# Performance work log

Measured on AMD Instinct MI355X. Metric: run time of the kernel, lower is better.

## Reference

```python
import jax, jax.numpy as jnp
import numpy as np

B, S, D = 64, 14, 2048   # batch, enc_image_size, encoder_dim
A, H, E = 512, 512, 512  # attention_dim, lstm_size, embedding_size
V, L = 10000, 20         # vocab_size, max caption length (T = L-1 decode steps)


def setup_inputs() -> dict:
    key = jax.random.key(0)
    ks = jax.random.split(key, 24)
    p = lambda k, shape: jax.random.normal(k, shape, jnp.float32) * 0.02
    features = jax.random.normal(ks[0], (B, S, S, D), jnp.float32)
    captions = jax.random.randint(ks[1], (B, L), 0, V)
    # sorted descending lengths in [2, L], max forced to L so T_dec = L-1
    lengths = jnp.sort(jax.random.randint(ks[2], (B,), 2, L + 1))[::-1]
    lengths = lengths.at[0].set(L)
    return {
        'features': features, 'captions': captions, 'lengths': lengths,
        'emb': p(ks[3], (V, E)),
        'W_ih': p(ks[4], (4 * H, D + E)), 'b_ih': p(ks[5], (4 * H,)),
        'W_hh': p(ks[6], (4 * H, H)), 'b_hh': p(ks[7], (4 * H,)),
        'h_fc_w': p(ks[8], (H, D)), 'h_fc_b': p(ks[9], (H,)),
        'c_fc_w': p(ks[10], (H, D)), 'c_fc_b': p(ks[11], (H,)),
        'f_beta_w': p(ks[12], (D, H)), 'f_beta_b': p(ks[13], (D,)),
        'cls_w': p(ks[14], (V, H)), 'cls_b': p(ks[15], (V,)),
        'enc_w': p(ks[16], (A, D)), 'enc_b': p(ks[17], (A,)),
        'dec_w': p(ks[18], (A, H)), 'dec_b': p(ks[19], (A,)),
        'att_w': p(ks[20], (1, A)), 'att_b': p(ks[21], (1,)),
    }


def reference(features, captions, lengths, emb, W_ih, b_ih, W_hh, b_hh,
              h_fc_w, h_fc_b, c_fc_w, c_fc_b, f_beta_w, f_beta_b,
              cls_w, cls_b, enc_w, enc_b, dec_w, dec_b, att_w, att_b):
    feats = features.reshape(features.shape[0], -1, features.shape[-1])  # (B,P,D)
    emb_seq = emb[captions]                                              # (B,L,E)
    mean_f = feats.mean(axis=1)
    h = mean_f @ h_fc_w.T + h_fc_b
    c = mean_f @ c_fc_w.T + c_fc_b
    dec_len = lengths - 1
    T = captions.shape[1] - 1
    # attention encoder projection is time-invariant: hoist out of the loop
    att1 = jnp.einsum('bpd,ad->bpa', feats, enc_w) + enc_b               # (B,P,A)

    def step(carry, xs):
        h, c = carry
        x_emb, t = xs
        att2 = h @ dec_w.T + dec_b                                       # (B,A)
        e = jnp.einsum('bpa,a->bp', jax.nn.relu(att1 + att2[:, None, :]), att_w[0]) + att_b[0]
        alpha = jax.nn.softmax(e, axis=1)                                # (B,P)
        awe = jnp.einsum('bp,bpd->bd', alpha, feats)
        gate = jax.nn.sigmoid(h @ f_beta_w.T + f_beta_b)
        awe = gate * awe
        x = jnp.concatenate([x_emb, awe], axis=1)                        # (B,E+D)
        gates = x @ W_ih.T + b_ih + h @ W_hh.T + b_hh                    # torch gate order i,f,g,o
        i, f, g, o = jnp.split(gates, 4, axis=1)
        c2 = jax.nn.sigmoid(f) * c + jax.nn.sigmoid(i) * jnp.tanh(g)
        h2 = jax.nn.sigmoid(o) * jnp.tanh(c2)
        y = h2 @ cls_w.T + cls_b                                         # dropout = eval identity
        active = (t < dec_len)[:, None]
        return (h2, c2), (jnp.where(active, y, 0.0), jnp.where(active, alpha, 0.0))

    xs = (jnp.swapaxes(emb_seq[:, :T], 0, 1), jnp.arange(T))
    (_, _), (y_pred, alphas) = jax.lax.scan(step, (h, c), xs)
    return jnp.swapaxes(y_pred, 0, 1), jnp.swapaxes(alphas, 0, 1)
```

## Files before the change

kernel.cpp:

```cpp
#include <hip/hip_runtime.h>
#include <math.h>

typedef __attribute__((ext_vector_type(8))) short bf16x8;
typedef __attribute__((ext_vector_type(8))) unsigned short u16x8;
typedef __attribute__((ext_vector_type(4))) float f32x4;

#define NB 64
#define NP 196
#define ND 2048
#define NA 512
#define NH 512
#define NE 512
#define NV 10000
#define NT 19
#define NKX 3072
#define NROW (NB*NP)
#define NVP 10112
#define MROW 1280
#define PP 200

__device__ __forceinline__ unsigned short f2bu(float f){
    unsigned int u; __builtin_memcpy(&u, &f, 4);
    u = (u + 0x7FFFu + ((u >> 16) & 1u)) >> 16;
    return (unsigned short)u;
}
__device__ __forceinline__ float b2f(short s){
    unsigned int u = ((unsigned int)(unsigned short)s) << 16;
    float f; __builtin_memcpy(&f, &u, 4); return f;
}
__device__ __forceinline__ float sigm(float x){ return 1.f/(1.f + __expf(-x)); }

__device__ __forceinline__ void gll16(const void* g, void* l){
    __builtin_amdgcn_global_load_lds(
        (const __attribute__((address_space(1))) void*)g,
        (__attribute__((address_space(3))) void*)l, 16, 0, 0);
}


__global__ void k_cast4(const float4* __restrict__ src, ushort4* __restrict__ dst, int n4){
    int stride = gridDim.x * blockDim.x;
    for (int i = blockIdx.x*blockDim.x + threadIdx.x; i < n4; i += stride){
        float4 v = src[i];
        ushort4 o = { f2bu(v.x), f2bu(v.y), f2bu(v.z), f2bu(v.w) };
        dst[i] = o;
    }
}

__global__ void k_wcat(const float* __restrict__ wih, const float* __restrict__ whh,
                       unsigned short* __restrict__ wcat){
    int j = blockIdx.x;
    int k = blockIdx.y*256 + threadIdx.x;
    float v = (k < 2560) ? wih[j*2560 + k] : whh[j*512 + (k - 2560)];
    wcat[j*NKX + k] = f2bu(v);
}

__global__ void k_tr(const float* __restrict__ feats,
                     unsigned short* __restrict__ fbf,
                     unsigned short* __restrict__ ftr,
                     float* __restrict__ meanf){
    __shared__ unsigned short sm[64][202];
    __shared__ float rsum[256];
    int dt = blockIdx.x;
    int b  = blockIdx.y;
    int tid = threadIdx.x;
    int d = tid & 63;
    int gd = dt*64 + d;
    float s = 0.f;
    for (int p = (tid >> 6); p < NP; p += 4){
        float v = feats[((size_t)(b*NP + p))*ND + gd];
        unsigned short u = f2bu(v);
        fbf[((size_t)(b*NP + p))*ND + gd] = u;
        sm[d][p] = u;
        s += v;
    }
    rsum[tid] = s;
    __syncthreads();
    if (tid < 64)
        meanf[b*ND + dt*64 + tid] =
            (rsum[tid] + rsum[tid+64] + rsum[tid+128] + rsum[tid+192]) * (1.f/196.f);
    for (int v = tid; v < 64*25; v += 256){
        int r = v/25, c = v - r*25;
        u16x8 o;
        #pragma unroll
        for (int j = 0; j < 8; j++){ int p = c*8 + j; o[j] = (p < NP) ? sm[r][p] : (unsigned short)0; }
        *(u16x8*)(ftr + ((size_t)(b*ND + dt*64 + r))*PP + c*8) = o;
    }
}

__global__ void k_hc0(const float* __restrict__ meanf,
                      const float* __restrict__ hw, const float* __restrict__ hb,
                      const float* __restrict__ cw, const float* __restrict__ cb,
                      unsigned short* __restrict__ hbf, float* __restrict__ cst){
    int sel = blockIdx.y;
    const float* wmat = sel ? cw : hw;
    const float* bias = sel ? cb : hb;
    int jg = blockIdx.x;
    int tid = threadIdx.x;
    int b = tid & 63, jj = tid >> 6;
    int j = jg*4 + jj;
    __shared__ float ml[64][33];
    __shared__ float wl[4][32];
    float acc = 0.f;
    for (int kc = 0; kc < ND; kc += 32){
        __syncthreads();
        #pragma unroll
        for (int q = 0; q < 8; q++){
            int lin = tid + q*256;
            int r = lin >> 5, kk = lin & 31;
            ml[r][kk] = meanf[r*ND + kc + kk];
        }
        if (tid < 128){ int r = tid >> 5, kk = tid & 31; wl[r][kk] = wmat[(jg*4 + r)*ND + kc + kk]; }
        __syncthreads();
        #pragma unroll
        for (int kk = 0; kk < 32; kk++) acc += ml[b][kk] * wl[jj][kk];
    }
    acc += bias[j];
    if (sel) cst[b*NH + j] = acc;
    else     hbf[b*NH + j] = f2bu(acc);
}

template<int K>
__device__ __forceinline__ void gemm128(const unsigned short* __restrict__ A,
                                        const unsigned short* __restrict__ B,
                                        int brow, int bcol, f32x4 acc[4][4]){
    __shared__ unsigned short As[128*32];
    __shared__ unsigned short Bs[128*32];
    int tid = threadIdx.x;
    int w = tid >> 6, l = tid & 63;
    int wr = (w >> 1) * 64, wc = (w & 1) * 64;
    int lr = l & 15, kg = (l >> 4) * 8;
    const unsigned short* ga0 = A + (size_t)(brow + (tid >> 2))*K + (tid & 3)*8;
    const unsigned short* gb0 = B + (size_t)(bcol + (tid >> 2))*K + (tid & 3)*8;
    for (int k0 = 0; k0 < K; k0 += 32){
        __syncthreads();
        gll16(ga0 + k0,            As + w*512);
        gll16(ga0 + (size_t)64*K + k0, As + 2048 + w*512);
        gll16(gb0 + k0,            Bs + w*512);
        gll16(gb0 + (size_t)64*K + k0, Bs + 2048 + w*512);
        __syncthreads();
        bf16x8 af[4], bfr[4];
        #pragma unroll
        for (int mi = 0; mi < 4; mi++)
            af[mi] = *(const bf16x8*)(As + (wr + mi*16 + lr)*32 + kg);
        #pragma unroll
        for (int ni = 0; ni < 4; ni++)
            bfr[ni] = *(const bf16x8*)(Bs + (wc + ni*16 + lr)*32 + kg);
        #pragma unroll
        for (int ni = 0; ni < 4; ni++){
            #pragma unroll
            for (int mi = 0; mi < 4; mi++)
                acc[mi][ni] = __builtin_amdgcn_mfma_f32_16x16x32_bf16(af[mi], bfr[ni], acc[mi][ni], 0, 0, 0);
        }
    }
}

__global__ void k_gemm_att1(const unsigned short* __restrict__ fbf,
                            const unsigned short* __restrict__ encw,
                            const float* __restrict__ enc_b,
                            unsigned short* __restrict__ att1){
    f32x4 acc[4][4] = {};
    int brow = blockIdx.x*128, bcol = blockIdx.y*128;
    gemm128<ND>(fbf, encw, brow, bcol, acc);
    int w = threadIdx.x >> 6, l = threadIdx.x & 63;
    int wr = (w >> 1) * 64, wc = (w & 1) * 64;
    int r0 = brow + wr + (l >> 4)*4;
    int c0 = bcol + wc + (l & 15);
    #pragma unroll
    for (int ni = 0; ni < 4; ni++){
        int col = c0 + ni*16;
        float eb = enc_b[col];
        #pragma unroll
        for (int mi = 0; mi < 4; mi++){
            #pragma unroll
            for (int r = 0; r < 4; r++)
                att1[(size_t)(r0 + mi*16 + r)*NA + col] = f2bu(acc[mi][ni][r] + eb);
        }
    }
}

__global__ void k_gemm_cls(const unsigned short* __restrict__ hsb,
                           const unsigned short* __restrict__ clsw,
                           const float* __restrict__ cls_b,
                           const int* __restrict__ lengths,
                           float* __restrict__ yout){
    f32x4 acc[4][4] = {};
    int brow = blockIdx.x*128, bcol = blockIdx.y*128;
    gemm128<NH>(hsb, clsw, brow, bcol, acc);
    int w = threadIdx.x >> 6, l = threadIdx.x & 63;
    int wr = (w >> 1) * 64, wc = (w & 1) * 64;
    int r0 = brow + wr + (l >> 4)*4;
    int c0 = bcol + wc + (l & 15);
    #pragma unroll
    for (int ni = 0; ni < 4; ni++){
        int col = c0 + ni*16;
        if (col >= NV) continue;
        float cb = cls_b[col];
        #pragma unroll
        for (int mi = 0; mi < 4; mi++){
            #pragma unroll
            for (int r = 0; r < 4; r++){
                int grow = r0 + mi*16 + r;
                if (grow >= NT*64) continue;
                int t = grow >> 6, bb = grow & 63;
                int active = t < (lengths[bb] - 1);
                yout[((size_t)bb*NT + t)*NV + col] = active ? (acc[mi][ni][r] + cb) : 0.f;
            }
        }
    }
}


__global__ void k_hproj(const unsigned short* __restrict__ hbf,
                        const unsigned short* __restrict__ hwb,
                        float* __restrict__ hp){
    int w = threadIdx.x >> 6, l = threadIdx.x & 63;
    int nt = blockIdx.x;
    int row = 16*w + (l & 15);
    int col = nt*16 + (l & 15);
    int kg = (l >> 4) * 8;
    f32x4 acc = {};
    for (int k0 = 0; k0 < NH; k0 += 32){
        bf16x8 af = *(const bf16x8*)(hbf + row*NH + k0 + kg);
        bf16x8 bv = *(const bf16x8*)(hwb + col*NH + k0 + kg);
        acc = __builtin_amdgcn_mfma_f32_16x16x32_bf16(af, bv, acc, 0, 0, 0);
    }
    int r0 = 16*w + (l >> 4)*4;
    #pragma unroll
    for (int r = 0; r < 4; r++)
        hp[(r0 + r)*2560 + col] = acc[r];
}

__global__ void k_e(const unsigned short* __restrict__ att1,
                    const float* __restrict__ hp, const float* __restrict__ dec_b,
                    const float* __restrict__ att_w, const float* __restrict__ att_b,
                    const float* __restrict__ emb, const int* __restrict__ captions,
                    const unsigned short* __restrict__ hbf,
                    unsigned short* __restrict__ xh, float* __restrict__ ews, int t){
    __shared__ float at2[NA];
    __shared__ float aw[NA];
    int b = blockIdx.x >> 2, pc = blockIdx.x & 3;
    int tid = threadIdx.x;
    for (int j = tid; j < NA; j += 256){
        at2[j] = hp[b*2560 + j] + dec_b[j];
        aw[j]  = att_w[j];
    }
    if (pc == 0){
        int cap = captions[b*20 + t];
        for (int k = tid; k < NE; k += 256) xh[b*NKX + k] = f2bu(emb[cap*NE + k]);
        for (int j = tid; j < NH; j += 256) xh[b*NKX + 2560 + j] = hbf[b*NH + j];
    }
    __syncthreads();
    int pl = tid >> 2, q = tid & 3;
    if (pl < 49){
        int p = pc*49 + pl;
        const unsigned short* arow = att1 + ((size_t)(b*NP + p))*NA + q*128;
        float s = 0.f;
        for (int a0 = 0; a0 < 128; a0 += 8){
            bf16x8 v = *(const bf16x8*)(arow + a0);
            #pragma unroll
            for (int e = 0; e < 8; e++){
                int a = q*128 + a0 + e;
                float x = b2f(v[e]) + at2[a];
                s += fmaxf(x, 0.f) * aw[a];
            }
        }
        s += __shfl_xor(s, 1);
        s += __shfl_xor(s, 2);
        if (q == 0) ews[b*NP + p] = s + att_b[0];
    }
}

__global__ void k_awe(const float* __restrict__ ews, const unsigned short* __restrict__ ftr,
                      const float* __restrict__ hp, const float* __restrict__ f_beta_b,
                      const int* __restrict__ lengths,
                      unsigned short* __restrict__ xh, float* __restrict__ alphas_out, int t){
    __shared__ float al[PP];
    __shared__ float red[256];
    int dc = blockIdx.x;
    int b  = blockIdx.y;
    int tid = threadIdx.x;
    float v = (tid < NP) ? ews[b*NP + tid] : -1e30f;
    red[tid] = v; __syncthreads();
    for (int s = 128; s > 0; s >>= 1){ if (tid < s) red[tid] = fmaxf(red[tid], red[tid+s]); __syncthreads(); }
    float m = red[0]; __syncthreads();
    float ev = (tid < NP) ? __expf(v - m) : 0.f;
    red[tid] = ev; __syncthreads();
    for (int s = 128; s > 0; s >>= 1){ if (tid < s) red[tid] += red[tid+s]; __syncthreads(); }
    float inv = 1.f / red[0];
    if (tid < NP) al[tid] = ev * inv;
    if (tid >= NP && tid < PP) al[tid] = 0.f;
    __syncthreads();
    if (dc == 0 && tid < NP){
        int active = t < (lengths[b] - 1);
        alphas_out[((size_t)b*NT + t)*NP + tid] = active ? al[tid] : 0.f;
    }
    int d = dc*256 + tid;
    const unsigned short* fr = ftr + ((size_t)(b*ND + d))*PP;
    float a0 = 0.f, a1 = 0.f, a2 = 0.f, a3 = 0.f;
    #pragma unroll
    for (int c = 0; c < 25; c++){
        bf16x8 vv = *(const bf16x8*)(fr + c*8);
        float* accp = (c & 3) == 0 ? &a0 : (c & 3) == 1 ? &a1 : (c & 3) == 2 ? &a2 : &a3;
        float s = 0.f;
        #pragma unroll
        for (int j = 0; j < 8; j++) s += al[c*8 + j] * b2f(vv[j]);
        *accp += s;
    }
    float acc = (a0 + a1) + (a2 + a3);
    float g = sigm(hp[b*2560 + 512 + d] + f_beta_b[d]);
    xh[b*NKX + 512 + d] = f2bu(g * acc);
}

__global__ void k_gates(const unsigned short* __restrict__ xh,
                        const unsigned short* __restrict__ wcat,
                        float* __restrict__ part){
    int w = threadIdx.x >> 6, l = threadIdx.x & 63;
    int nt = blockIdx.x;
    int s  = blockIdx.y;
    int row = 16*w + (l & 15);
    int col = nt*16 + (l & 15);
    int kg = (l >> 4) * 8;
    int kbase = s*384;
    f32x4 acc = {};
    for (int k0 = 0; k0 < 384; k0 += 32){
        bf16x8 af = *(const bf16x8*)(xh + row*NKX + kbase + k0 + kg);
        bf16x8 bv = *(const bf16x8*)(wcat + col*NKX + kbase + k0 + kg);
        acc = __builtin_amdgcn_mfma_f32_16x16x32_bf16(af, bv, acc, 0, 0, 0);
    }
    int r0 = 16*w + (l >> 4)*4;
    #pragma unroll
    for (int r = 0; r < 4; r++)
        part[(s*64 + r0 + r)*2048 + col] = acc[r];
}

__global__ void k_lstm(const float* __restrict__ part,
                       const float* __restrict__ b_ih, const float* __restrict__ b_hh,
                       float* __restrict__ cst, unsigned short* __restrict__ hbf,
                       unsigned short* __restrict__ hsb, int t){
    int idx = blockIdx.x*256 + threadIdx.x;
    int b = idx >> 9, j = idx & 511;
    float gi = b_ih[j]        + b_hh[j];
    float gf = b_ih[512 + j]  + b_hh[512 + j];
    float gg = b_ih[1024 + j] + b_hh[1024 + j];
    float go = b_ih[1536 + j] + b_hh[1536 + j];
    #pragma unroll
    for (int s = 0; s < 8; s++){
        const float* pb = part + (s*64 + b)*2048;
        gi += pb[j]; gf += pb[512 + j]; gg += pb[1024 + j]; go += pb[1536 + j];
    }
    float c = cst[b*NH + j];
    float c2 = sigm(gf)*c + sigm(gi)*tanhf(gg);
    float h2 = sigm(go)*tanhf(c2);
    cst[b*NH + j] = c2;
    unsigned short hb16 = f2bu(h2);
    hbf[b*NH + j] = hb16;
    hsb[((t - 1)*64 + b)*NH + j] = hb16;
}


extern "C" void kernel_launch(void* const* d_in, const int* in_sizes, int n_in,
                              void* d_out, int out_size, void* d_ws, size_t ws_size,
                              hipStream_t stream){
    const float* features = (const float*)d_in[0];
    const int*   captions = (const int*)d_in[1];
    const int*   lengths  = (const int*)d_in[2];
    const float* emb      = (const float*)d_in[3];
    const float* W_ih     = (const float*)d_in[4];
    const float* b_ih     = (const float*)d_in[5];
    const float* W_hh     = (const float*)d_in[6];
    const float* b_hh     = (const float*)d_in[7];
    const float* h_fc_w   = (const float*)d_in[8];
    const float* h_fc_b   = (const float*)d_in[9];
    const float* c_fc_w   = (const float*)d_in[10];
    const float* c_fc_b   = (const float*)d_in[11];
    const float* f_beta_w = (const float*)d_in[12];
    const float* f_beta_b = (const float*)d_in[13];
    const float* cls_w    = (const float*)d_in[14];
    const float* cls_b    = (const float*)d_in[15];
    const float* enc_w    = (const float*)d_in[16];
    const float* enc_b    = (const float*)d_in[17];
    const float* dec_w    = (const float*)d_in[18];
    const float* dec_b    = (const float*)d_in[19];
    const float* att_w    = (const float*)d_in[20];
    const float* att_b    = (const float*)d_in[21];

    char* w = (char*)d_ws;
    size_t off = 0;
    auto alloc = [&](size_t bytes)->char*{
        char* p = w + off;
        off += (bytes + 255) & ~(size_t)255;
        return p;
    };
    unsigned short* fbf   = (unsigned short*)alloc((size_t)NROW*ND*2);
    unsigned short* ftr   = (unsigned short*)alloc((size_t)NB*ND*PP*2);
    unsigned short* att1  = (unsigned short*)alloc((size_t)NROW*NA*2);
    unsigned short* encwb = (unsigned short*)alloc((size_t)NA*ND*2);
    unsigned short* hwb   = (unsigned short*)alloc((size_t)2560*NH*2);
    unsigned short* wcat  = (unsigned short*)alloc((size_t)2048*NKX*2);
    unsigned short* clswb = (unsigned short*)alloc((size_t)NVP*NH*2);
    unsigned short* hsb   = (unsigned short*)alloc((size_t)MROW*NH*2);
    unsigned short* hbf   = (unsigned short*)alloc((size_t)64*NH*2);
    unsigned short* xh    = (unsigned short*)alloc((size_t)64*NKX*2);
    float* meanf = (float*)alloc((size_t)64*ND*4);
    float* cst   = (float*)alloc((size_t)64*NH*4);
    float* hp    = (float*)alloc((size_t)64*2560*4);
    float* ews   = (float*)alloc((size_t)64*NP*4);
    float* part  = (float*)alloc((size_t)8*64*2048*4);

    float* yout = (float*)d_out;
    float* alphas_out = yout + (size_t)NB*NT*NV;

    k_tr<<<dim3(32, 64), 256, 0, stream>>>(features, fbf, ftr, meanf);
    k_cast4<<<1024, 256, 0, stream>>>((const float4*)enc_w, (ushort4*)encwb, NA*ND/4);
    k_cast4<<<256, 256, 0, stream>>>((const float4*)dec_w, (ushort4*)hwb, 512*512/4);
    k_cast4<<<1024, 256, 0, stream>>>((const float4*)f_beta_w, (ushort4*)(hwb + 512*512), 2048*512/4);
    k_wcat<<<dim3(2048, 12), 256, 0, stream>>>(W_ih, W_hh, wcat);
    k_cast4<<<2048, 256, 0, stream>>>((const float4*)cls_w, (ushort4*)clswb, NV*NH/4);
    hipMemsetAsync(clswb + (size_t)NV*NH, 0, (size_t)(NVP - NV)*NH*2, stream);
    hipMemsetAsync(hsb + (size_t)NT*64*NH, 0, (size_t)(MROW - NT*64)*NH*2, stream);
    k_hc0<<<dim3(128, 2), 256, 0, stream>>>(meanf, h_fc_w, h_fc_b, c_fc_w, c_fc_b, hbf, cst);
    k_gemm_att1<<<dim3(98, 4), 256, 0, stream>>>(fbf, encwb, enc_b, att1);

    for (int t = 0; t < NT; t++){
        if (t > 0)
            k_lstm<<<128, 256, 0, stream>>>(part, b_ih, b_hh, cst, hbf, hsb, t);
        k_hproj<<<160, 256, 0, stream>>>(hbf, hwb, hp);
        k_e<<<256, 256, 0, stream>>>(att1, hp, dec_b, att_w, att_b, emb, captions, hbf, xh, ews, t);
        k_awe<<<dim3(8, 64), 256, 0, stream>>>(ews, ftr, hp, f_beta_b, lengths, xh, alphas_out, t);
        k_gates<<<dim3(128, 8), 256, 0, stream>>>(xh, wcat, part);
    }
    k_lstm<<<128, 256, 0, stream>>>(part, b_ih, b_hh, cst, hbf, hsb, NT);
    k_gemm_cls<<<dim3(10, 79), 256, 0, stream>>>(hsb, clswb, cls_b, lengths, yout);
}
```

Measured before the change: 1.236 ms.

## Fuse per-step LSTM/attention kernels and merge weight-cast preprocessing launches

Result: slower. 2.082 ms (+68.4%).

```diff
diff --git a/kernel.cpp b/kernel.cpp
--- a/kernel.cpp
+++ b/kernel.cpp
@@ -24,8 +24,8 @@
     u = (u + 0x7FFFu + ((u >> 16) & 1u)) >> 16;
     return (unsigned short)u;
 }
-__device__ __forceinline__ float b2f(short s){
-    unsigned int u = ((unsigned int)(unsigned short)s) << 16;
+__device__ __forceinline__ float b2f(unsigned short s){
+    unsigned int u = ((unsigned int)s) << 16;
     float f; __builtin_memcpy(&f, &u, 4); return f;
 }
 __device__ __forceinline__ float sigm(float x){ return 1.f/(1.f + __expf(-x)); }
@@ -37,60 +37,104 @@
 }
 
 
-__global__ void k_cast4(const float4* __restrict__ src, ushort4* __restrict__ dst, int n4){
-    int stride = gridDim.x * blockDim.x;
-    for (int i = blockIdx.x*blockDim.x + threadIdx.x; i < n4; i += stride){
-        float4 v = src[i];
-        ushort4 o = { f2bu(v.x), f2bu(v.y), f2bu(v.z), f2bu(v.w) };
-        dst[i] = o;
-    }
-}
-
-__global__ void k_wcat(const float* __restrict__ wih, const float* __restrict__ whh,
-                       unsigned short* __restrict__ wcat){
-    int j = blockIdx.x;
-    int k = blockIdx.y*256 + threadIdx.x;
-    float v = (k < 2560) ? wih[j*2560 + k] : whh[j*512 + (k - 2560)];
-    wcat[j*NKX + k] = f2bu(v);
-}
-
-__global__ void k_tr(const float* __restrict__ feats,
-                     unsigned short* __restrict__ fbf,
-                     unsigned short* __restrict__ ftr,
-                     float* __restrict__ meanf){
-    __shared__ unsigned short sm[64][202];
-    __shared__ float rsum[256];
-    int dt = blockIdx.x;
+__global__ void k_prep(const float4* __restrict__ enc_w, const float4* __restrict__ dec_w,
+                       const float4* __restrict__ f_beta_w, const float4* __restrict__ W_ih,
+                       const float4* __restrict__ W_hh, const float4* __restrict__ cls_w,
+                       ushort4* __restrict__ encwb, ushort4* __restrict__ hwb,
+                       ushort4* __restrict__ wcat, ushort4* __restrict__ clswb,
+                       ushort4* __restrict__ hsb_pad){
+    const int n0 = NA*ND/4;
+    const int n1 = 2560*512/4;
+    const int n2 = 2048*3072/4;
+    const int n3 = NVP*NH/4;
+    const int n4 = 64*512/4;
+    const int total = n0+n1+n2+n3+n4;
+    int stride = gridDim.x*blockDim.x;
+    for (int i = blockIdx.x*blockDim.x + threadIdx.x; i < total; i += stride){
+        int idx = i;
+        float4 v; ushort4 o;
+        if (idx < n0){
+            v = enc_w[idx];
+            o = (ushort4){ f2bu(v.x), f2bu(v.y), f2bu(v.z), f2bu(v.w) };
+            encwb[idx] = o; continue;
+        }
+        idx -= n0;
+        if (idx < n1){
+            v = (idx < 512*512/4) ? dec_w[idx] : f_beta_w[idx - 512*512/4];
+            o = (ushort4){ f2bu(v.x), f2bu(v.y), f2bu(v.z), f2bu(v.w) };
+            hwb[idx] = o; continue;
+        }
+        idx -= n1;
+        if (idx < n2){
+            int j = idx / 768, kk4 = idx - j*768;
+            v = (kk4 < 640) ? W_ih[(size_t)j*640 + kk4] : W_hh[(size_t)j*128 + (kk4 - 640)];
+            o = (ushort4){ f2bu(v.x), f2bu(v.y), f2bu(v.z), f2bu(v.w) };
+            wcat[idx] = o; continue;
+        }
+        idx -= n2;
+        if (idx < n3){
+            if (idx < NV*NH/4){
+                v = cls_w[idx];
+                o = (ushort4){ f2bu(v.x), f2bu(v.y), f2bu(v.z), f2bu(v.w) };
+            } else o = (ushort4){0,0,0,0};
+            clswb[idx] = o; continue;
+        }
+        idx -= n3;
+        hsb_pad[idx] = (ushort4){0,0,0,0};
+    }
+}
+
+__global__ void k_tr2(const float* __restrict__ feats,
+                      unsigned short* __restrict__ fbf,
+                      unsigned short* __restrict__ ftr,
+                      float* __restrict__ meanf){
+    __shared__ unsigned short sm[64][260];
+    __shared__ float4 msum[256];
+    int dc = blockIdx.x;
     int b  = blockIdx.y;
     int tid = threadIdx.x;
-    int d = tid & 63;
-    int gd = dt*64 + d;
-    float s = 0.f;
-    for (int p = (tid >> 6); p < NP; p += 4){
-        float v = feats[((size_t)(b*NP + p))*ND + gd];
-        unsigned short u = f2bu(v);
-        fbf[((size_t)(b*NP + p))*ND + gd] = u;
-        sm[d][p] = u;
-        s += v;
-    }
-    rsum[tid] = s;
+    int c4 = tid & 63;
+    int rq = tid >> 6;
+    int D0 = dc*256;
+    float4 acc = {0.f,0.f,0.f,0.f};
+    for (int pc = 0; pc < 4; pc++){
+        __syncthreads();
+        #pragma unroll
+        for (int i = 0; i < 16; i++){
+            int rl = rq + 4*i;
+            int p = pc*64 + rl;
+            float4 v = {0.f,0.f,0.f,0.f};
+            if (p < NP) v = *(const float4*)(feats + ((size_t)(b*NP + p))*ND + D0 + c4*4);
+            acc.x += v.x; acc.y += v.y; acc.z += v.z; acc.w += v.w;
+            ushort4 u4 = { f2bu(v.x), f2bu(v.y), f2bu(v.z), f2bu(v.w) };
+            if (p < NP) *(ushort4*)(fbf + ((size_t)(b*NP + p))*ND + D0 + c4*4) = u4;
+            *(ushort4*)&sm[rl][c4*4] = u4;
+        }
+        __syncthreads();
+        int gmax = (pc == 3) ? 1 : 8;
+        for (int g = 0; g < gmax; g++){
+            u16x8 o;
+            #pragma unroll
+            for (int k = 0; k < 8; k++) o[k] = sm[g*8 + k][tid];
+            *(u16x8*)(ftr + ((size_t)(b*ND + D0 + tid))*PP + pc*64 + g*8) = o;
+        }
+    }
+    msum[tid] = acc;
     __syncthreads();
-    if (tid < 64)
-        meanf[b*ND + dt*64 + tid] =
-            (rsum[tid] + rsum[tid+64] + rsum[tid+128] + rsum[tid+192]) * (1.f/196.f);
-    for (int v = tid; v < 64*25; v += 256){
-        int r = v/25, c = v - r*25;
-        u16x8 o;
-        #pragma unroll
-        for (int j = 0; j < 8; j++){ int p = c*8 + j; o[j] = (p < NP) ? sm[r][p] : (unsigned short)0; }
-        *(u16x8*)(ftr + ((size_t)(b*ND + dt*64 + r))*PP + c*8) = o;
+    if (tid < 64){
+        float4 s0 = msum[tid], s1 = msum[tid+64], s2 = msum[tid+128], s3 = msum[tid+192];
+        float4 tot = { (s0.x+s1.x)+(s2.x+s3.x), (s0.y+s1.y)+(s2.y+s3.y),
+                       (s0.z+s1.z)+(s2.z+s3.z), (s0.w+s1.w)+(s2.w+s3.w) };
+        tot.x *= (1.f/196.f); tot.y *= (1.f/196.f); tot.z *= (1.f/196.f); tot.w *= (1.f/196.f);
+        *(float4*)(meanf + (size_t)b*ND + D0 + tid*4) = tot;
     }
 }
 
 __global__ void k_hc0(const float* __restrict__ meanf,
                       const float* __restrict__ hw, const float* __restrict__ hb,
                       const float* __restrict__ cw, const float* __restrict__ cb,
-                      unsigned short* __restrict__ hbf, float* __restrict__ cst){
+                      unsigned short* __restrict__ hbf, float* __restrict__ cst,
+                      unsigned short* __restrict__ xh){
     int sel = blockIdx.y;
     const float* wmat = sel ? cw : hw;
     const float* bias = sel ? cb : hb;
@@ -116,7 +160,7 @@
     }
     acc += bias[j];
     if (sel) cst[b*NH + j] = acc;
-    else     hbf[b*NH + j] = f2bu(acc);
+    else { unsigned short u = f2bu(acc); hbf[b*NH + j] = u; xh[b*NKX + 2560 + j] = u; }
 }
 
 template<int K>
@@ -133,9 +177,9 @@
     const unsigned short* gb0 = B + (size_t)(bcol + (tid >> 2))*K + (tid & 3)*8;
     for (int k0 = 0; k0 < K; k0 += 32){
         __syncthreads();
-        gll16(ga0 + k0,            As + w*512);
+        gll16(ga0 + k0,                As + w*512);
         gll16(ga0 + (size_t)64*K + k0, As + 2048 + w*512);
-        gll16(gb0 + k0,            Bs + w*512);
+        gll16(gb0 + k0,                Bs + w*512);
         gll16(gb0 + (size_t)64*K + k0, Bs + 2048 + w*512);
         __syncthreads();
         bf16x8 af[4], bfr[4];
@@ -210,133 +254,211 @@
 }
 
 
-__global__ void k_hproj(const unsigned short* __restrict__ hbf,
+__global__ void k_step1(const float* __restrict__ part,
+                        const float* __restrict__ b_ih, const float* __restrict__ b_hh,
+                        float* __restrict__ cst, unsigned short* __restrict__ hbf,
+                        unsigned short* __restrict__ hsb, unsigned short* __restrict__ xh,
                         const unsigned short* __restrict__ hwb,
-                        float* __restrict__ hp){
-    int w = threadIdx.x >> 6, l = threadIdx.x & 63;
-    int nt = blockIdx.x;
-    int row = 16*w + (l & 15);
-    int col = nt*16 + (l & 15);
-    int kg = (l >> 4) * 8;
-    f32x4 acc = {};
-    for (int k0 = 0; k0 < NH; k0 += 32){
-        bf16x8 af = *(const bf16x8*)(hbf + row*NH + k0 + kg);
-        bf16x8 bv = *(const bf16x8*)(hwb + col*NH + k0 + kg);
-        acc = __builtin_amdgcn_mfma_f32_16x16x32_bf16(af, bv, acc, 0, 0, 0);
-    }
-    int r0 = 16*w + (l >> 4)*4;
-    #pragma unroll
-    for (int r = 0; r < 4; r++)
-        hp[(r0 + r)*2560 + col] = acc[r];
-}
-
-__global__ void k_e(const unsigned short* __restrict__ att1,
-                    const float* __restrict__ hp, const float* __restrict__ dec_b,
-                    const float* __restrict__ att_w, const float* __restrict__ att_b,
-                    const float* __restrict__ emb, const int* __restrict__ captions,
-                    const unsigned short* __restrict__ hbf,
-                    unsigned short* __restrict__ xh, float* __restrict__ ews, int t){
-    __shared__ float at2[NA];
-    __shared__ float aw[NA];
-    int b = blockIdx.x >> 2, pc = blockIdx.x & 3;
+                        const float* __restrict__ dec_b,
+                        const unsigned short* __restrict__ att1,
+                        const float* __restrict__ att_w, const float* __restrict__ att_b,
+                        const float* __restrict__ emb, const int* __restrict__ captions,
+                        const int* __restrict__ lengths,
+                        float* __restrict__ alw, float* __restrict__ alphas, int t){
+    __shared__ float hls[512];
+    __shared__ float at2s[512];
+    __shared__ float aws[512];
+    __shared__ float red[256];
+    int b = blockIdx.x, tid = threadIdx.x;
+    if (t > 0){
+        for (int j = tid; j < 512; j += 256){
+            float gi = b_ih[j]        + b_hh[j];
+            float gf = b_ih[512 + j]  + b_hh[512 + j];
+            float gg = b_ih[1024 + j] + b_hh[1024 + j];
+            float go = b_ih[1536 + j] + b_hh[1536 + j];
+            #pragma unroll
+            for (int s = 0; s < 8; s++){
+                const float* pb = part + (size_t)(s*64 + b)*2048;
+                gi += pb[j]; gf += pb[512 + j]; gg += pb[1024 + j]; go += pb[1536 + j];
+            }
+            float c = cst[b*NH + j];
+            float c2 = sigm(gf)*c + sigm(gi)*tanhf(gg);
+            float h2 = sigm(go)*tanhf(c2);
+            cst[b*NH + j] = c2;
+            hls[j] = h2;
+            unsigned short u = f2bu(h2);
+            hbf[b*NH + j] = u;
+            xh[b*NKX + 2560 + j] = u;
+            hsb[((size_t)(t - 1)*64 + b)*NH + j] = u;
+        }
+    } else {
+        for (int j = tid; j < 512; j += 256) hls[j] = b2f(hbf[b*NH + j]);
+    }
+    int cap = captions[b*20 + t];
+    for (int k = tid; k < 512; k += 256){
+        xh[b*NKX + k] = f2bu(emb[(size_t)cap*NE + k]);
+        aws[k] = att_w[k];
+    }
+    __syncthreads();
+    {
+        float acc0 = dec_b[tid], acc1 = dec_b[tid + 256];
+        const unsigned short* w0 = hwb + (size_t)tid*512;
+        const unsigned short* w1 = hwb + (size_t)(tid + 256)*512;
+        for (int j = 0; j < 512; j += 8){
+            bf16x8 x0 = *(const bf16x8*)(w0 + j);
+            bf16x8 x1 = *(const bf16x8*)(w1 + j);
+            #pragma unroll
+            for (int e = 0; e < 8; e++){
+                float hv = hls[j + e];
+                acc0 += hv * b2f((unsigned short)x0[e]);
+                acc1 += hv * b2f((unsigned short)x1[e]);
+            }
+        }
+        at2s[tid] = acc0; at2s[tid + 256] = acc1;
+    }
+    __syncthreads();
+    float s = -1e30f;
+    if (tid < NP){
+        const unsigned short* arow = att1 + ((size_t)(b*NP + tid))*NA;
+        float acc = att_b[0];
+        for (int a0 = 0; a0 < 512; a0 += 8){
+            bf16x8 v = *(const bf16x8*)(arow + a0);
+            #pragma unroll
+            for (int e = 0; e < 8; e++){
+                float x = b2f((unsigned short)v[e]) + at2s[a0 + e];
+                acc += fmaxf(x, 0.f) * aws[a0 + e];
+            }
+        }
+        s = acc;
+    }
+    red[tid] = s; __syncthreads();
+    for (int st = 128; st > 0; st >>= 1){ if (tid < st) red[tid] = fmaxf(red[tid], red[tid+st]); __syncthreads(); }
+    float m = red[0]; __syncthreads();
+    float ev = (tid < NP) ? __expf(s - m) : 0.f;
+    red[tid] = ev; __syncthreads();
+    for (int st = 128; st > 0; st >>= 1){ if (tid < st) red[tid] += red[tid+st]; __syncthreads(); }
+    float inv = 1.f / red[0];
+    float al = ev * inv;
+    if (tid < PP) alw[b*PP + tid] = (tid < NP) ? al : 0.f;
+    if (tid < NP){
+        int active = t < (lengths[b] - 1);
+        alphas[((size_t)b*NT + t)*NP + tid] = active ? al : 0.f;
+    }
+}
+
+__global__ void k_step2(const unsigned short* __restrict__ hbf,
+                        const unsigned short* __restrict__ hwb,
+                        const float* __restrict__ f_beta_b,
+                        const float* __restrict__ alw,
+                        const unsigned short* __restrict__ ftr,
+                        float* __restrict__ hbeta, float* __restrict__ awer){
     int tid = threadIdx.x;
-    for (int j = tid; j < NA; j += 256){
-        at2[j] = hp[b*2560 + j] + dec_b[j];
-        aw[j]  = att_w[j];
-    }
-    if (pc == 0){
-        int cap = captions[b*20 + t];
-        for (int k = tid; k < NE; k += 256) xh[b*NKX + k] = f2bu(emb[cap*NE + k]);
-        for (int j = tid; j < NH; j += 256) xh[b*NKX + 2560 + j] = hbf[b*NH + j];
-    }
-    __syncthreads();
-    int pl = tid >> 2, q = tid & 3;
-    if (pl < 49){
-        int p = pc*49 + pl;
-        const unsigned short* arow = att1 + ((size_t)(b*NP + p))*NA + q*128;
-        float s = 0.f;
-        for (int a0 = 0; a0 < 128; a0 += 8){
-            bf16x8 v = *(const bf16x8*)(arow + a0);
-            #pragma unroll
-            for (int e = 0; e < 8; e++){
-                int a = q*128 + a0 + e;
-                float x = b2f(v[e]) + at2[a];
-                s += fmaxf(x, 0.f) * aw[a];
-            }
-        }
-        s += __shfl_xor(s, 1);
-        s += __shfl_xor(s, 2);
-        if (q == 0) ews[b*NP + p] = s + att_b[0];
-    }
-}
-
-__global__ void k_awe(const float* __restrict__ ews, const unsigned short* __restrict__ ftr,
-                      const float* __restrict__ hp, const float* __restrict__ f_beta_b,
-                      const int* __restrict__ lengths,
-                      unsigned short* __restrict__ xh, float* __restrict__ alphas_out, int t){
-    __shared__ float al[PP];
-    __shared__ float red[256];
-    int dc = blockIdx.x;
-    int b  = blockIdx.y;
-    int tid = threadIdx.x;
-    float v = (tid < NP) ? ews[b*NP + tid] : -1e30f;
-    red[tid] = v; __syncthreads();
-    for (int s = 128; s > 0; s >>= 1){ if (tid < s) red[tid] = fmaxf(red[tid], red[tid+s]); __syncthreads(); }
-    float m = red[0]; __syncthreads();
-    float ev = (tid < NP) ? __expf(v - m) : 0.f;
-    red[tid] = ev; __syncthreads();
-    for (int s = 128; s > 0; s >>= 1){ if (tid < s) red[tid] += red[tid+s]; __syncthreads(); }
-    float inv = 1.f / red[0];
-    if (tid < NP) al[tid] = ev * inv;
-    if (tid >= NP && tid < PP) al[tid] = 0.f;
-    __syncthreads();
-    if (dc == 0 && tid < NP){
-        int active = t < (lengths[b] - 1);
-        alphas_out[((size_t)b*NT + t)*NP + tid] = active ? al[tid] : 0.f;
-    }
-    int d = dc*256 + tid;
-    const unsigned short* fr = ftr + ((size_t)(b*ND + d))*PP;
-    float a0 = 0.f, a1 = 0.f, a2 = 0.f, a3 = 0.f;
-    #pragma unroll
-    for (int c = 0; c < 25; c++){
-        bf16x8 vv = *(const bf16x8*)(fr + c*8);
-        float* accp = (c & 3) == 0 ? &a0 : (c & 3) == 1 ? &a1 : (c & 3) == 2 ? &a2 : &a3;
-        float s = 0.f;
-        #pragma unroll
-        for (int j = 0; j < 8; j++) s += al[c*8 + j] * b2f(vv[j]);
-        *accp += s;
-    }
-    float acc = (a0 + a1) + (a2 + a3);
-    float g = sigm(hp[b*2560 + 512 + d] + f_beta_b[d]);
-    xh[b*NKX + 512 + d] = f2bu(g * acc);
-}
-
-__global__ void k_gates(const unsigned short* __restrict__ xh,
-                        const unsigned short* __restrict__ wcat,
-                        float* __restrict__ part){
-    int w = threadIdx.x >> 6, l = threadIdx.x & 63;
+    if (blockIdx.x < 128){
+        int nt = blockIdx.x;
+        int w = tid >> 6, l = tid & 63;
+        int row = 16*w + (l & 15);
+        int col = nt*16 + (l & 15);
+        int kg = (l >> 4) * 8;
+        f32x4 acc = {};
+        for (int k0 = 0; k0 < NH; k0 += 32){
+            bf16x8 af = *(const bf16x8*)(hbf + row*NH + k0 + kg);
+            bf16x8 bv = *(const bf16x8*)(hwb + (size_t)(512 + col)*NH + k0 + kg);
+            acc = __builtin_amdgcn_mfma_f32_16x16x32_bf16(af, bv, acc, 0, 0, 0);
+        }
+        int r0 = 16*w + (l >> 4)*4;
+        float fb = f_beta_b[col];
+        #pragma unroll
+        for (int r = 0; r < 4; r++)
+            hbeta[(size_t)(r0 + r)*2048 + col] = acc[r] + fb;
+    } else {
+        __shared__ float als[PP];
+        int id2 = blockIdx.x - 128;
+        int b = id2 >> 3, dc = id2 & 7;
+        if (tid < PP) als[tid] = alw[b*PP + tid];
+        __syncthreads();
+        int d = dc*256 + tid;
+        const unsigned short* fr = ftr + ((size_t)(b*ND + d))*PP;
+        float a0 = 0.f, a1 = 0.f, a2 = 0.f, a3 = 0.f;
+        #pragma unroll
+        for (int c = 0; c < 25; c++){
+            bf16x8 vv = *(const bf16x8*)(fr + c*8);
+            float ss = 0.f;
+            #pragma unroll
+            for (int j = 0; j < 8; j++) ss += als[c*8 + j] * b2f((unsigned short)vv[j]);
+            if ((c & 3) == 0) a0 += ss; else if ((c & 3) == 1) a1 += ss;
+            else if ((c & 3) == 2) a2 += ss; else a3 += ss;
+        }
+        awer[(size_t)b*2048 + d] = (a0 + a1) + (a2 + a3);
+    }
+}
+
+#define AST 392
+__global__ void k_gates2(const unsigned short* __restrict__ xh,
+                         const float* __restrict__ hbeta, const float* __restrict__ awer,
+                         const unsigned short* __restrict__ wcat,
+                         float* __restrict__ part){
+    __shared__ unsigned short As[64*AST];
+    __shared__ unsigned short Bs[128*32];
     int nt = blockIdx.x;
     int s  = blockIdx.y;
-    int row = 16*w + (l & 15);
-    int col = nt*16 + (l & 15);
-    int kg = (l >> 4) * 8;
-    int kbase = s*384;
-    f32x4 acc = {};
+    int tid = threadIdx.x;
+    int w = tid >> 6, l = tid & 63;
+    #pragma unroll 4
+    for (int rr = 0; rr < 16; rr++){
+        int r = (tid >> 6) + rr*4;
+        #pragma unroll
+        for (int c = 0; c < 6; c++){
+            int kk = c*64 + (tid & 63);
+            int k = s*384 + kk;
+            unsigned short v;
+            if (k < 512 || k >= 2560) v = xh[r*NKX + k];
+            else {
+                int d = k - 512;
+                float g = sigm(hbeta[(size_t)r*2048 + d]);
+                v = f2bu(g * awer[(size_t)r*2048 + d]);
+            }
+            As[r*AST + kk] = v;
+        }
+    }
+    int wc = w*32;
+    int lr = l & 15, kg = (l >> 4) * 8;
+    const unsigned short* gb0 = wcat + (size_t)(nt*128 + (tid >> 2))*NKX + s*384 + (tid & 3)*8;
+    f32x4 acc[4][2] = {};
     for (int k0 = 0; k0 < 384; k0 += 32){
-        bf16x8 af = *(const bf16x8*)(xh + row*NKX + kbase + k0 + kg);
-        bf16x8 bv = *(const bf16x8*)(wcat + col*NKX + kbase + k0 + kg);
-        acc = __builtin_amdgcn_mfma_f32_16x16x32_bf16(af, bv, acc, 0, 0, 0);
-    }
-    int r0 = 16*w + (l >> 4)*4;
+        __syncthreads();
+        gll16(gb0 + k0,                 Bs + w*512);
+        gll16(gb0 + (size_t)64*NKX + k0, Bs + 2048 + w*512);
+        __syncthreads();
+        bf16x8 af[4], bfr[2];
+        #pragma unroll
+        for (int mi = 0; mi < 4; mi++)
+            af[mi] = *(const bf16x8*)(As + (mi*16 + lr)*AST + k0 + kg);
+        #pragma unroll
+        for (int ni = 0; ni < 2; ni++)
+            bfr[ni] = *(const bf16x8*)(Bs + (wc + ni*16 + lr)*32 + kg);
+        #pragma unroll
+        for (int ni = 0; ni < 2; ni++){
+            #pragma unroll
+            for (int mi = 0; mi < 4; mi++)
+                acc[mi][ni] = __builtin_amdgcn_mfma_f32_16x16x32_bf16(af[mi], bfr[ni], acc[mi][ni], 0, 0, 0);
+        }
+    }
+    int r0 = (l >> 4)*4;
     #pragma unroll
-    for (int r = 0; r < 4; r++)
-        part[(s*64 + r0 + r)*2048 + col] = acc[r];
-}
-
-__global__ void k_lstm(const float* __restrict__ part,
-                       const float* __restrict__ b_ih, const float* __restrict__ b_hh,
-                       float* __restrict__ cst, unsigned short* __restrict__ hbf,
-                       unsigned short* __restrict__ hsb, int t){
+    for (int ni = 0; ni < 2; ni++){
+        int col = nt*128 + wc + ni*16 + (l & 15);
+        #pragma unroll
+        for (int mi = 0; mi < 4; mi++){
+            #pragma unroll
+            for (int r = 0; r < 4; r++)
+                part[(size_t)(s*64 + mi*16 + r0 + r)*2048 + col] = acc[mi][ni][r];
+        }
+    }
+}
+
+__global__ void k_lstm_fin(const float* __restrict__ part,
+                           const float* __restrict__ b_ih, const float* __restrict__ b_hh,
+                           float* __restrict__ cst, unsigned short* __restrict__ hsb){
     int idx = blockIdx.x*256 + threadIdx.x;
     int b = idx >> 9, j = idx & 511;
     float gi = b_ih[j]        + b_hh[j];
@@ -345,16 +467,13 @@
     float go = b_ih[1536 + j] + b_hh[1536 + j];
     #pragma unroll
     for (int s = 0; s < 8; s++){
-        const float* pb = part + (s*64 + b)*2048;
+        const float* pb = part + (size_t)(s*64 + b)*2048;
         gi += pb[j]; gf += pb[512 + j]; gg += pb[1024 + j]; go += pb[1536 + j];
     }
     float c = cst[b*NH + j];
     float c2 = sigm(gf)*c + sigm(gi)*tanhf(gg);
     float h2 = sigm(go)*tanhf(c2);
-    cst[b*NH + j] = c2;
-    unsigned short hb16 = f2bu(h2);
-    hbf[b*NH + j] = hb16;
-    hsb[((t - 1)*64 + b)*NH + j] = hb16;
+    hsb[((size_t)(NT - 1)*64 + b)*NH + j] = f2bu(h2);
 }
 
 
@@ -403,32 +522,30 @@
     unsigned short* xh    = (unsigned short*)alloc((size_t)64*NKX*2);
     float* meanf = (float*)alloc((size_t)64*ND*4);
     float* cst   = (float*)alloc((size_t)64*NH*4);
-    float* hp    = (float*)alloc((size_t)64*2560*4);
-    float* ews   = (float*)alloc((size_t)64*NP*4);
+    float* hbeta = (float*)alloc((size_t)64*2048*4);
+    float* alw   = (float*)alloc((size_t)64*PP*4);
+    float* awer  = (float*)alloc((size_t)64*2048*4);
     float* part  = (float*)alloc((size_t)8*64*2048*4);
 
     float* yout = (float*)d_out;
     float* alphas_out = yout + (size_t)NB*NT*NV;
 
-    k_tr<<<dim3(32, 64), 256, 0, stream>>>(features, fbf, ftr, meanf);
-    k_cast4<<<1024, 256, 0, stream>>>((const float4*)enc_w, (ushort4*)encwb, NA*ND/4);
-    k_cast4<<<256, 256, 0, stream>>>((const float4*)dec_w, (ushort4*)hwb, 512*512/4);
-    k_cast4<<<1024, 256, 0, stream>>>((const float4*)f_beta_w, (ushort4*)(hwb + 512*512), 2048*512/4);
-    k_wcat<<<dim3(2048, 12), 256, 0, stream>>>(W_ih, W_hh, wcat);
-    k_cast4<<<2048, 256, 0, stream>>>((const float4*)cls_w, (ushort4*)clswb, NV*NH/4);
-    hipMemsetAsync(clswb + (size_t)NV*NH, 0, (size_t)(NVP - NV)*NH*2, stream);
-    hipMemsetAsync(hsb + (size_t)NT*64*NH, 0, (size_t)(MROW - NT*64)*NH*2, stream);
-    k_hc0<<<dim3(128, 2), 256, 0, stream>>>(meanf, h_fc_w, h_fc_b, c_fc_w, c_fc_b, hbf, cst);
+    k_tr2<<<dim3(8, 64), 256, 0, stream>>>(features, fbf, ftr, meanf);
+    k_prep<<<1024, 256, 0, stream>>>((const float4*)enc_w, (const float4*)dec_w,
+                                     (const float4*)f_beta_w, (const float4*)W_ih,
+                                     (const float4*)W_hh, (const float4*)cls_w,
+                                     (ushort4*)encwb, (ushort4*)hwb, (ushort4*)wcat,
+                                     (ushort4*)clswb, (ushort4*)(hsb + (size_t)NT*64*NH));
+    k_hc0<<<dim3(128, 2), 256, 0, stream>>>(meanf, h_fc_w, h_fc_b, c_fc_w, c_fc_b, hbf, cst, xh);
     k_gemm_att1<<<dim3(98, 4), 256, 0, stream>>>(fbf, encwb, enc_b, att1);
 
     for (int t = 0; t < NT; t++){
-        if (t > 0)
-            k_lstm<<<128, 256, 0, stream>>>(part, b_ih, b_hh, cst, hbf, hsb, t);
-        k_hproj<<<160, 256, 0, stream>>>(hbf, hwb, hp);
-        k_e<<<256, 256, 0, stream>>>(att1, hp, dec_b, att_w, att_b, emb, captions, hbf, xh, ews, t);
-        k_awe<<<dim3(8, 64), 256, 0, stream>>>(ews, ftr, hp, f_beta_b, lengths, xh, alphas_out, t);
-        k_gates<<<dim3(128, 8), 256, 0, stream>>>(xh, wcat, part);
-    }
-    k_lstm<<<128, 256, 0, stream>>>(part, b_ih, b_hh, cst, hbf, hsb, NT);
+        k_step1<<<64, 256, 0, stream>>>(part, b_ih, b_hh, cst, hbf, hsb, xh,
+                                        hwb, dec_b, att1, att_w, att_b,
+                                        emb, captions, lengths, alw, alphas_out, t);
+        k_step2<<<640, 256, 0, stream>>>(hbf, hwb, f_beta_b, alw, ftr, hbeta, awer);
+        k_gates2<<<dim3(16, 8), 256, 0, stream>>>(xh, hbeta, awer, wcat, part);
+    }
+    k_lstm_fin<<<128, 256, 0, stream>>>(part, b_ih, b_hh, cst, hsb);
     k_gemm_cls<<<dim3(10, 79), 256, 0, stream>>>(hsb, clswb, cls_b, lengths, yout);
 }
```
